# Kernel tuning notes

Measured on AMD Instinct MI355X. Metric: run time of the kernel, lower is better.

## Reference

```python
import jax, jax.numpy as jnp
import numpy as np

THRESHOLD = 0.2
NEG_POS_RATIO = 3
ALPHA = 1.0
B, M, P, C = 64, 50, 24564, 2


def cxcy_to_xy(c):
    return jnp.concatenate([c[..., :2] - c[..., 2:] / 2, c[..., :2] + c[..., 2:] / 2], axis=-1)


def xy_to_cxcy(x):
    return jnp.concatenate([(x[..., :2] + x[..., 2:]) / 2, x[..., 2:] - x[..., :2]], axis=-1)


def cxcy_to_gcxgcy(c, p):
    # SSD encoding: offsets scaled by 10, sizes (log) scaled by 5
    return jnp.concatenate([(c[..., :2] - p[..., :2]) / (p[..., 2:] / 10.0),
                            jnp.log(c[..., 2:] / p[..., 2:]) * 5.0], axis=-1)


def jaccard(a, b):
    # a: (M,4) xy boxes, b: (P,4) xy boxes -> (M,P) IoU
    lt = jnp.maximum(a[:, None, :2], b[None, :, :2])
    rb = jnp.minimum(a[:, None, 2:], b[None, :, 2:])
    inter = jnp.prod(jnp.clip(rb - lt, 0.0), axis=-1)
    area_a = jnp.prod(a[:, 2:] - a[:, :2], axis=-1)
    area_b = jnp.prod(b[:, 2:] - b[:, :2], axis=-1)
    return inter / (area_a[:, None] + area_b[None, :] - inter)


def setup_inputs() -> dict:
    key = jax.random.key(0)
    k1, k2, k3, k4, k5, k6 = jax.random.split(key, 6)
    predicted_locs = jax.random.normal(k1, (B, P, 4), dtype=jnp.float32)
    predicted_scores = jax.random.normal(k2, (B, P, C), dtype=jnp.float32)
    # valid GT corner boxes in [0,1]: x2>x1, y2>y1
    xy1 = jax.random.uniform(k3, (B, M, 2), minval=0.0, maxval=0.75)
    wh = jax.random.uniform(k4, (B, M, 2), minval=0.05, maxval=0.25)
    boxes = jnp.concatenate([xy1, xy1 + wh], axis=-1).astype(jnp.float32)
    # priors in cxcywh with positive sizes
    pc = jax.random.uniform(k5, (P, 2), minval=0.0, maxval=1.0)
    pwh = jax.random.uniform(k6, (P, 2), minval=0.02, maxval=0.3)
    priors_cxcy = jnp.concatenate([pc, pwh], axis=-1).astype(jnp.float32)
    return {"predicted_locs": predicted_locs, "predicted_scores": predicted_scores,
            "boxes": boxes, "priors_cxcy": priors_cxcy}


def reference(predicted_locs, predicted_scores, boxes, priors_cxcy):
    n_priors = priors_cxcy.shape[0]
    priors_xy = cxcy_to_xy(priors_cxcy)

    def assign(boxes_i):  # boxes_i: (M,4) xy
        overlap = jaccard(boxes_i, priors_xy)  # (M,P)
        overlap_for_each_prior = overlap.max(axis=0)        # (P,)
        object_for_each_prior = overlap.argmax(axis=0)      # (P,)
        prior_for_each_object = overlap.argmax(axis=1)      # (M,)
        # force each object's best prior to be assigned to that object
        object_for_each_prior = object_for_each_prior.at[prior_for_each_object].set(jnp.arange(boxes_i.shape[0]))
        overlap_for_each_prior = overlap_for_each_prior.at[prior_for_each_object].set(1.0)
        labels = jnp.where(overlap_for_each_prior < THRESHOLD, 0, 1).astype(jnp.int32)
        true_locs = cxcy_to_gcxgcy(xy_to_cxcy(boxes_i[object_for_each_prior]), priors_cxcy)
        return labels, true_locs

    true_classes, true_locs = jax.vmap(assign)(boxes)  # (B,P), (B,P,4)
    pos = true_classes != 0                            # (B,P)
    n_pos = pos.sum(axis=1)                            # (B,)
    total_pos = n_pos.sum().astype(jnp.float32)

    # L1Loss(mean) over the positive-prior coordinates
    loc_abs = jnp.abs(predicted_locs - true_locs)
    loc_loss = jnp.sum(loc_abs * pos[..., None]) / (total_pos * 4.0)

    # per-prior cross entropy
    logp = jax.nn.log_softmax(predicted_scores, axis=-1)
    conf_all = -jnp.take_along_axis(logp, true_classes[..., None].astype(jnp.int32), axis=-1)[..., 0]  # (B,P)
    conf_pos_sum = jnp.sum(conf_all * pos)

    # hard negative mining: zero positives, sort descending, take top 3*n_pos per image
    conf_neg = jnp.where(pos, 0.0, conf_all)
    conf_neg_sorted = -jnp.sort(-conf_neg, axis=1)
    ranks = jnp.arange(n_priors)[None, :]
    hard = ranks < (NEG_POS_RATIO * n_pos)[:, None]
    conf_hard_sum = jnp.sum(conf_neg_sorted * hard)

    conf_loss = (conf_hard_sum + conf_pos_sum) / total_pos
    return conf_loss + ALPHA * loc_loss
```

## Files before the change

kernel.cpp:

```cpp
#include <hip/hip_runtime.h>
#include <math.h>

#define BB 64
#define MM 50
#define PP 24564
#define NBLK 96
#define THRESH 0.2f
#define P4 (PP / 4)
#define SLACK 64u
#define NCH 24
#define WMARG 0.151f
#define RCPM 8u
#define SELCH 8
#define SCH4 ((P4 + SELCH - 1) / SELCH)
#define CAP PP

__device__ __forceinline__ float l1loc(float4 bxm, float4 pc, float4 pl) {
    float cx = (bxm.x + bxm.z) * 0.5f, cy = (bxm.y + bxm.w) * 0.5f;
    float w = bxm.z - bxm.x, h = bxm.w - bxm.y;
    float g0 = (cx - pc.x) / (pc.z * 0.1f);
    float g1 = (cy - pc.y) / (pc.w * 0.1f);
    float g2 = logf(w / pc.z) * 5.0f;
    float g3 = logf(h / pc.w) * 5.0f;
    return fabsf(pl.x - g0) + fabsf(pl.y - g1) + fabsf(pl.z - g2) + fabsf(pl.w - g3);
}

__global__ void k_init(int* __restrict__ ghist, int* __restrict__ ghist2,
                       int* __restrict__ gcur, unsigned long long* __restrict__ Lm) {
    int i = blockIdx.x * 256 + threadIdx.x;
    if (i < BB * 2048) ghist[i] = 0;
    if (i < BB * 1024) ghist2[i] = 0;
    if (i < BB) gcur[i] = 0;
    if (i < BB * MM) Lm[i] = 0x00000000FFFFFFFFull;
}

__global__ void k_main(const float4* __restrict__ boxes,
                       const float4* __restrict__ pr_cxcy,
                       const float4* __restrict__ plocs,
                       const float2* __restrict__ scores,
                       unsigned long long* __restrict__ Lm,
                       float* __restrict__ bestv,
                       int* __restrict__ bmv,
                       float* __restrict__ confneg,
                       int* __restrict__ ghist,
                       int* __restrict__ npos_part,
                       float* __restrict__ cpos_part,
                       float* __restrict__ loc_part) {
    int b = blockIdx.y;
    int p = blockIdx.x * 256 + threadIdx.x;
    int tid = threadIdx.x;
    __shared__ unsigned long long smax[MM];
    __shared__ int shist[2048];
    __shared__ int si[256];
    __shared__ float s1[256], s2[256];
    for (int i = tid; i < 2048; i += 256) shist[i] = 0;
    if (tid < MM) smax[tid] = 0ull;
    __syncthreads();

    const float4* boxb = boxes + b * MM;
    int np = 0;
    float cpos = 0.0f, lloc = 0.0f;
    if (p < PP) {
        float4 pc = pr_cxcy[p];
        float px1 = pc.x - pc.z * 0.5f, py1 = pc.y - pc.w * 0.5f;
        float px2 = pc.x + pc.z * 0.5f, py2 = pc.y + pc.w * 0.5f;
        float pa = (px2 - px1) * (py2 - py1);
        float binter = 0.0f, bdenom = 1.0f;
        int bm = 0;
        float4 bbm = boxb[0];
        #pragma unroll 5
        for (int m = 0; m < MM; ++m) {
            float4 bxm = boxb[m];
            float am = (bxm.z - bxm.x) * (bxm.w - bxm.y);
            float lx = fmaxf(bxm.x, px1), ly = fmaxf(bxm.y, py1);
            float rx = fminf(bxm.z, px2), ry = fminf(bxm.w, py2);
            float iw = fmaxf(rx - lx, 0.0f), ih = fmaxf(ry - ly, 0.0f);
            float inter = iw * ih;
            float den = am + pa - inter;
            float l = inter * bdenom, r = binter * den;
            if (l > r) { binter = inter; bdenom = den; bm = m; bbm = bxm; }
        }
        float q = binter / bdenom;
        size_t idx = (size_t)b * PP + p;
        bestv[idx] = q;
        bmv[idx] = bm;
        unsigned long long key =
            ((unsigned long long)__float_as_uint(q) << 32) | (unsigned int)(~p);
        atomicMax(&smax[bm], key);
        bool pos = (q >= THRESH);
        float2 sc = scores[idx];
        float mx = fmaxf(sc.x, sc.y);
        float lse = mx + logf(expf(sc.x - mx) + expf(sc.y - mx));
        float conf = pos ? (lse - sc.y) : (lse - sc.x);
        float ck = pos ? 0.0f : conf;
        confneg[idx] = ck;
        atomicAdd(&shist[__float_as_uint(ck) >> 20], 1);
        if (pos) {
            np = 1;
            cpos = conf;
            lloc = l1loc(bbm, pc, plocs[idx]);
        }
    }
    si[tid] = np; s1[tid] = cpos; s2[tid] = lloc;
    __syncthreads();
    for (int s = 128; s > 0; s >>= 1) {
        if (tid < s) {
            si[tid] += si[tid + s];
            s1[tid] += s1[tid + s];
            s2[tid] += s2[tid + s];
        }
        __syncthreads();
    }
    if (tid == 0) {
        int o = b * NBLK + blockIdx.x;
        npos_part[o] = si[0];
        cpos_part[o] = s1[0];
        loc_part[o] = s2[0];
    }
    if (tid < MM) {
        unsigned long long v = smax[tid];
        if (v) atomicMax(&Lm[b * MM + tid], v);
    }
    for (int i = tid; i < 2048; i += 256) {
        int c = shist[i];
        if (c) atomicAdd(&ghist[b * 2048 + i], c);
    }
}

__global__ void k_bpo3(const float4* __restrict__ boxes,
                       const float4* __restrict__ pr_cxcy,
                       const float* __restrict__ bestv,
                       unsigned long long* __restrict__ Lm) {
    int b = blockIdx.y, c = blockIdx.x, tid = threadIdx.x;
    __shared__ unsigned thr[MM];
    __shared__ unsigned long long smax[MM];
    __shared__ unsigned sminthr;
    if (tid < MM) {
        unsigned long long L = Lm[b * MM + tid];
        smax[tid] = L;
        unsigned hi = (unsigned)(L >> 32);
        thr[tid] = (hi > SLACK) ? hi - SLACK : 0u;
    }
    __syncthreads();
    if (tid == 0) {
        unsigned mt = 0xFFFFFFFFu;
        for (int j = 0; j < MM; ++j) mt = min(mt, thr[j]);
        sminthr = mt;
    }
    __syncthreads();
    unsigned minthr = sminthr;
    volatile unsigned long long* vsm = smax;
    const float4* boxb = boxes + b * MM;
    const float4* bv4 = (const float4*)(bestv + (size_t)b * PP);
    int i = c * 256 + tid;
    if (i < P4) {
        float4 qv = bv4[i];
        float vv[4] = {qv.x, qv.y, qv.z, qv.w};
        #pragma unroll
        for (int e = 0; e < 4; ++e) {
            unsigned qb = __float_as_uint(vv[e]);
            if (qb < minthr) continue;
            int p = 4 * i + e;
            float4 pc = pr_cxcy[p];
            float px1 = pc.x - pc.z * 0.5f, py1 = pc.y - pc.w * 0.5f;
            float px2 = pc.x + pc.z * 0.5f, py2 = pc.y + pc.w * 0.5f;
            float pa = (px2 - px1) * (py2 - py1);
            for (int j = 0; j < MM; ++j) {
                if (qb < thr[j]) continue;
                float4 bxm = boxb[j];
                if (pc.x < bxm.x - WMARG || pc.x > bxm.z + WMARG ||
                    pc.y < bxm.y - WMARG || pc.y > bxm.w + WMARG) continue;
                float am = (bxm.z - bxm.x) * (bxm.w - bxm.y);
                float lx = fmaxf(bxm.x, px1), ly = fmaxf(bxm.y, py1);
                float rx = fminf(bxm.z, px2), ry = fminf(bxm.w, py2);
                float iw = fmaxf(rx - lx, 0.0f), ih = fmaxf(ry - ly, 0.0f);
                float inter = iw * ih;
                float den = am + pa - inter;
                float qa = inter * __builtin_amdgcn_rcpf(den);
                unsigned hi = (unsigned)(vsm[j] >> 32);
                if (__float_as_uint(qa) + RCPM < hi) continue;
                float q = inter / den;
                unsigned long long key =
                    ((unsigned long long)__float_as_uint(q) << 32) | (unsigned int)(~p);
                if (key > vsm[j]) atomicMax(&smax[j], key);
            }
        }
    }
    __syncthreads();
    if (tid < MM) atomicMax(&Lm[b * MM + tid], smax[tid]);
}

__device__ __forceinline__ float block_sum(float v, float* fred, int tid) {
    fred[tid] = v;
    __syncthreads();
    for (int s = 128; s > 0; s >>= 1) {
        if (tid < s) fred[tid] += fred[tid + s];
        __syncthreads();
    }
    float r = fred[0];
    __syncthreads();
    return r;
}

template <int NB>
__device__ __forceinline__ void suffix_find(const int* __restrict__ h, int K, int tid,
                                            int* iscr, int* bcast, int slot) {
    const int c = NB / 256;
    const int base = tid * c;
    int tsum = 0;
    #pragma unroll
    for (int i = 0; i < c; ++i) tsum += h[base + i];
    iscr[tid] = tsum;
    __syncthreads();
    int val = tsum;
    for (int off = 1; off < 256; off <<= 1) {
        int other = (tid + off < 256) ? iscr[tid + off] : 0;
        __syncthreads();
        val += other;
        iscr[tid] = val;
        __syncthreads();
    }
    int acc = val - tsum;
    int best = -1, cg = 0;
    for (int i = base + c - 1; i >= base; --i) {
        int s = acc + h[i];
        if (s >= K) { best = i; cg = acc; break; }
        acc = s;
    }
    iscr[tid] = best;
    __syncthreads();
    for (int s2 = 128; s2 > 0; s2 >>= 1) {
        if (tid < s2) iscr[tid] = max(iscr[tid], iscr[tid + s2]);
        __syncthreads();
    }
    int gbest = iscr[0];
    __syncthreads();
    if (best == gbest && best >= 0) { bcast[slot] = gbest; bcast[slot + 1] = cg; }
    __syncthreads();
}

__global__ void k_selKF(const float4* __restrict__ boxes,
                        const float4* __restrict__ pr_cxcy,
                        const float4* __restrict__ plocs,
                        const float2* __restrict__ scores,
                        const unsigned long long* __restrict__ Lm,
                        const float* __restrict__ bestv,
                        const int* __restrict__ bmv,
                        float* __restrict__ confneg,
                        const int* __restrict__ ghist,
                        const int* __restrict__ npos_part,
                        int4* __restrict__ selp,
                        int* __restrict__ npfix,
                        float* __restrict__ cposfix,
                        float* __restrict__ llocfix) {
    int b = blockIdx.x, tid = threadIdx.x;
    __shared__ int h[2048];
    __shared__ int iscr[256];
    __shared__ int bcast[8];
    __shared__ int s_dnp;
    for (int i = tid; i < 2048; i += 256) h[i] = ghist[b * 2048 + i];
    __syncthreads();
    if (tid < 64) {
        int fp = -1;
        if (tid < MM) fp = (int)(~(unsigned)(Lm[b * MM + tid] & 0xFFFFFFFFull));
        bool active = (tid < MM);
        for (int m2 = 0; m2 < MM; ++m2) {
            int v = __shfl(fp, m2);
            if (m2 > tid && v == fp) active = false;
        }
        int dnp = 0;
        float dcp = 0.0f, dll = 0.0f;
        if (active) {
            size_t idx = (size_t)b * PP + fp;
            float bo = bestv[idx];
            bool npold = (bo >= THRESH);
            float4 pc = pr_cxcy[fp];
            float4 pl = plocs[idx];
            float llnew = l1loc(boxes[b * MM + tid], pc, pl);
            if (npold) {
                dll = llnew - l1loc(boxes[b * MM + bmv[idx]], pc, pl);
            } else {
                float2 sc = scores[idx];
                float mx = fmaxf(sc.x, sc.y);
                float lse = mx + logf(expf(sc.x - mx) + expf(sc.y - mx));
                dnp = 1;
                dcp = lse - sc.y;
                dll = llnew;
                float cold = confneg[idx];
                atomicAdd(&h[(int)(__float_as_uint(cold) >> 20)], -1);
                atomicAdd(&h[0], 1);
                confneg[idx] = 0.0f;
            }
        }
        #pragma unroll
        for (int off = 32; off > 0; off >>= 1) {
            dnp += __shfl_xor(dnp, off);
            dcp += __shfl_xor(dcp, off);
            dll += __shfl_xor(dll, off);
        }
        if (tid == 0) {
            s_dnp = dnp;
            npfix[b] = dnp; cposfix[b] = dcp; llocfix[b] = dll;
        }
    }
    __syncthreads();
    iscr[tid] = (tid < NBLK) ? npos_part[b * NBLK + tid] : 0;
    __syncthreads();
    for (int s = 128; s > 0; s >>= 1) {
        if (tid < s) iscr[tid] += iscr[tid + s];
        __syncthreads();
    }
    int npos = iscr[0] + s_dnp;
    __syncthreads();
    long long Kl = 3LL * npos;
    int K = (Kl > PP) ? PP : (int)Kl;
    if (K == 0) {
        if (tid == 0) selp[b] = make_int4(0, -1, 0, 0);
        return;
    }
    suffix_find<2048>(h, K, tid, iscr, bcast, 0);
    if (tid == 0) {
        int b1 = bcast[0];
        selp[b] = make_int4(K, b1, K - bcast[1], h[b1]);
    }
}

__global__ void k_selA(const float* __restrict__ confneg,
                       const int4* __restrict__ selp,
                       float* __restrict__ saP,
                       int* __restrict__ ghist2,
                       int* __restrict__ gcur,
                       float* __restrict__ gstore) {
    int b = blockIdx.y, c = blockIdx.x, tid = threadIdx.x;
    __shared__ float fred[256];
    __shared__ int h2[1024];
    __shared__ float sstore[SCH4 * 4];
    __shared__ int scnt, sbase;
    for (int i = tid; i < 1024; i += 256) h2[i] = 0;
    if (tid == 0) scnt = 0;
    __syncthreads();
    int4 sp = selp[b];
    int b1 = sp.y;
    float sa = 0.0f;
    if (b1 >= 0) {
        const float4* cn4 = (const float4*)(confneg + (size_t)b * PP);
        int i1 = min((c + 1) * SCH4, P4);
        for (int i = c * SCH4 + tid; i < i1; i += 256) {
            float4 q = cn4[i];
            float vv[4] = {q.x, q.y, q.z, q.w};
            #pragma unroll
            for (int j = 0; j < 4; ++j) {
                unsigned k = __float_as_uint(vv[j]);
                int t11 = (int)(k >> 20);
                if (t11 > b1) sa += vv[j];
                else if (t11 == b1) {
                    atomicAdd(&h2[(k >> 10) & 1023], 1);
                    int ix = atomicAdd(&scnt, 1);
                    sstore[ix] = vv[j];
                }
            }
        }
    }
    __syncthreads();
    if (tid == 0 && scnt > 0) sbase = atomicAdd(&gcur[b], scnt);
    __syncthreads();
    int n = scnt;
    for (int i = tid; i < n; i += 256)
        gstore[(size_t)b * CAP + sbase + i] = sstore[i];
    for (int i = tid; i < 1024; i += 256) {
        int v = h2[i];
        if (v) atomicAdd(&ghist2[b * 1024 + i], v);
    }
    float Sa = block_sum(sa, fred, tid);
    if (tid == 0) saP[b * SELCH + c] = Sa;
}

__global__ void k_selB(const int4* __restrict__ selp,
                       const float* __restrict__ saP,
                       const int* __restrict__ ghist2,
                       const float* __restrict__ gstore,
                       float* __restrict__ chard) {
    int b = blockIdx.x, tid = threadIdx.x;
    __shared__ int h[1024];
    __shared__ float fred[256];
    __shared__ int iscr[256];
    __shared__ int bcast[8];
    __shared__ float sSa;
    int4 sp = selp[b];
    if (sp.x == 0) {
        if (tid == 0) chard[b] = 0.0f;
        return;
    }
    int b1 = sp.y, K1 = sp.z, h1cnt = sp.w;
    if (tid == 0) {
        float s = 0.0f;
        for (int j = 0; j < SELCH; ++j) s += saP[b * SELCH + j];
        sSa = s;
    }
    for (int i = tid; i < 1024; i += 256) h[i] = ghist2[b * 1024 + i];
    __syncthreads();
    float Sa = sSa;
    suffix_find<1024>(h, K1, tid, iscr, bcast, 0);
    int b2 = bcast[0];
    int K2 = K1 - bcast[1];
    unsigned top21 = ((unsigned)b1 << 10) | (unsigned)b2;
    __syncthreads();

    const float* gs = gstore + (size_t)b * CAP;
    for (int i = tid; i < 1024; i += 256) h[i] = 0;
    __syncthreads();
    float sb = 0.0f;
    for (int i = tid; i < h1cnt; i += 256) {
        float v = gs[i];
        unsigned k = __float_as_uint(v);
        int n10 = (int)((k >> 10) & 1023);
        if (n10 > b2) sb += v;
        else if (n10 == b2) atomicAdd(&h[k & 1023], 1);
    }
    float Sb = block_sum(sb, fred, tid);
    suffix_find<1024>(h, K2, tid, iscr, bcast, 2);
    int b3 = bcast[2];
    int K3 = K2 - bcast[3];
    float sc = 0.0f;
    for (int i = tid; i < h1cnt; i += 256) {
        float v = gs[i];
        unsigned k = __float_as_uint(v);
        if ((k >> 10) == top21 && (k & 1023) > (unsigned)b3) sc += v;
    }
    float Sc = block_sum(sc, fred, tid);
    if (tid == 0) {
        unsigned kstar = (top21 << 10) | (unsigned)b3;
        chard[b] = Sa + Sb + Sc + (float)K3 * __uint_as_float(kstar);
    }
}

__global__ void k_final(const int* __restrict__ npos_part,
                        const float* __restrict__ cpos_part,
                        const float* __restrict__ loc_part,
                        const float* __restrict__ chard,
                        const int* __restrict__ npfix,
                        const float* __restrict__ cposfix,
                        const float* __restrict__ llocfix,
                        float* __restrict__ out) {
    __shared__ int si[256];
    __shared__ float s1[256], s2[256], s3[256];
    int tn = 0; float tc = 0.0f, tl = 0.0f, th = 0.0f;
    for (int i = threadIdx.x; i < BB * NBLK; i += 256) {
        tn += npos_part[i];
        tc += cpos_part[i];
        tl += loc_part[i];
    }
    if (threadIdx.x < BB) {
        th = chard[threadIdx.x];
        tn += npfix[threadIdx.x];
        tc += cposfix[threadIdx.x];
        tl += llocfix[threadIdx.x];
    }
    si[threadIdx.x] = tn; s1[threadIdx.x] = tc; s2[threadIdx.x] = tl; s3[threadIdx.x] = th;
    __syncthreads();
    for (int s = 128; s > 0; s >>= 1) {
        if (threadIdx.x < s) {
            si[threadIdx.x] += si[threadIdx.x + s];
            s1[threadIdx.x] += s1[threadIdx.x + s];
            s2[threadIdx.x] += s2[threadIdx.x + s];
            s3[threadIdx.x] += s3[threadIdx.x + s];
        }
        __syncthreads();
    }
    if (threadIdx.x == 0) {
        float tp = (float)si[0];
        out[0] = (s3[0] + s1[0]) / tp + s2[0] / (tp * 4.0f);
    }
}

extern "C" void kernel_launch(void* const* d_in, const int* in_sizes, int n_in,
                              void* d_out, int out_size, void* d_ws, size_t ws_size,
                              hipStream_t stream) {
    const float4* plocs   = (const float4*)d_in[0];
    const float2* scores  = (const float2*)d_in[1];
    const float4* boxes   = (const float4*)d_in[2];
    const float4* priors  = (const float4*)d_in[3];
    float* out = (float*)d_out;

    char* ws = (char*)d_ws;
    size_t off = 0;
    auto alloc = [&](size_t bytes) -> void* {
        void* p = ws + off;
        off += (bytes + 255) & ~(size_t)255;
        return p;
    };
    float*              confneg = (float*) alloc((size_t)BB * PP * 4);
    float*              bestv   = (float*) alloc((size_t)BB * PP * 4);
    int*                bmv     = (int*)   alloc((size_t)BB * PP * 4);
    int*                ghist   = (int*)   alloc((size_t)BB * 2048 * 4);
    int*                ghist2  = (int*)   alloc((size_t)BB * 1024 * 4);
    unsigned long long* Lm      = (unsigned long long*)alloc((size_t)BB * MM * 8);
    int*                npos_p  = (int*)   alloc((size_t)BB * NBLK * 4);
    float*              cpos_p  = (float*) alloc((size_t)BB * NBLK * 4);
    float*              loc_p   = (float*) alloc((size_t)BB * NBLK * 4);
    float*              chard   = (float*) alloc((size_t)BB * 4);
    int*                npfix   = (int*)   alloc((size_t)BB * 4);
    float*              cposfix = (float*) alloc((size_t)BB * 4);
    float*              llocfix = (float*) alloc((size_t)BB * 4);
    int4*               selp    = (int4*)  alloc((size_t)BB * 16);
    float*              saP     = (float*) alloc((size_t)BB * SELCH * 4);
    int*                gcur    = (int*)   alloc((size_t)BB * 4);
    float*              gstore  = (float*) alloc((size_t)BB * CAP * 4);
    (void)ws_size; (void)in_sizes; (void)n_in; (void)out_size;

    k_init<<<512, 256, 0, stream>>>(ghist, ghist2, gcur, Lm);
    k_main<<<dim3(NBLK, BB), 256, 0, stream>>>(boxes, priors, plocs, scores,
                                               Lm, bestv, bmv, confneg, ghist,
                                               npos_p, cpos_p, loc_p);
    k_bpo3<<<dim3(NCH, BB), 256, 0, stream>>>(boxes, priors, bestv, Lm);
    k_selKF<<<BB, 256, 0, stream>>>(boxes, priors, plocs, scores, Lm, bestv, bmv,
                                    confneg, ghist, npos_p, selp,
                                    npfix, cposfix, llocfix);
    k_selA<<<dim3(SELCH, BB), 256, 0, stream>>>(confneg, selp, saP, ghist2, gcur, gstore);
    k_selB<<<BB, 256, 0, stream>>>(selp, saP, ghist2, gstore, chard);
    k_final<<<1, 256, 0, stream>>>(npos_p, cpos_p, loc_p, chard,
                                   npfix, cposfix, llocfix, out);
}
```

Before: 156.2 us.

## Cache GT boxes in LDS and sort thresholds for early-exit prior-object search

Both the IoU-assignment kernel and the per-object best-prior kernel now stage the image's GT boxes and their areas in shared memory instead of re-reading global memory each iteration. The second kernel sorts per-object thresholds by rank and computes a wavefront-wide max of the best-overlap values. A wave can then skip entirely, and each prior's object loop can break early once thresholds exceed that max. This trades some setup work (an O(M^2) rank sort and a shuffle reduction) for less divergent looping and fewer global box loads.

```diff
diff --git a/kernel.cpp b/kernel.cpp
--- a/kernel.cpp
+++ b/kernel.cpp
@@ -49,15 +49,21 @@
     int b = blockIdx.y;
     int p = blockIdx.x * 256 + threadIdx.x;
     int tid = threadIdx.x;
+    __shared__ float4 sbox[MM];
+    __shared__ float sarea[MM];
     __shared__ unsigned long long smax[MM];
     __shared__ int shist[2048];
     __shared__ int si[256];
     __shared__ float s1[256], s2[256];
     for (int i = tid; i < 2048; i += 256) shist[i] = 0;
-    if (tid < MM) smax[tid] = 0ull;
-    __syncthreads();
-
-    const float4* boxb = boxes + b * MM;
+    if (tid < MM) {
+        float4 bxt = boxes[b * MM + tid];
+        sbox[tid] = bxt;
+        sarea[tid] = (bxt.z - bxt.x) * (bxt.w - bxt.y);
+        smax[tid] = 0ull;
+    }
+    __syncthreads();
+
     int np = 0;
     float cpos = 0.0f, lloc = 0.0f;
     if (p < PP) {
@@ -67,18 +73,15 @@
         float pa = (px2 - px1) * (py2 - py1);
         float binter = 0.0f, bdenom = 1.0f;
         int bm = 0;
-        float4 bbm = boxb[0];
-        #pragma unroll 5
         for (int m = 0; m < MM; ++m) {
-            float4 bxm = boxb[m];
-            float am = (bxm.z - bxm.x) * (bxm.w - bxm.y);
+            float4 bxm = sbox[m];
             float lx = fmaxf(bxm.x, px1), ly = fmaxf(bxm.y, py1);
             float rx = fminf(bxm.z, px2), ry = fminf(bxm.w, py2);
             float iw = fmaxf(rx - lx, 0.0f), ih = fmaxf(ry - ly, 0.0f);
             float inter = iw * ih;
-            float den = am + pa - inter;
+            float den = sarea[m] + pa - inter;
             float l = inter * bdenom, r = binter * den;
-            if (l > r) { binter = inter; bdenom = den; bm = m; bbm = bxm; }
+            if (l > r) { binter = inter; bdenom = den; bm = m; }
         }
         float q = binter / bdenom;
         size_t idx = (size_t)b * PP + p;
@@ -98,7 +101,7 @@
         if (pos) {
             np = 1;
             cpos = conf;
-            lloc = l1loc(bbm, pc, plocs[idx]);
+            lloc = l1loc(sbox[bm], pc, plocs[idx]);
         }
     }
     si[tid] = np; s1[tid] = cpos; s2[tid] = lloc;
@@ -132,50 +135,69 @@
                        const float* __restrict__ bestv,
                        unsigned long long* __restrict__ Lm) {
     int b = blockIdx.y, c = blockIdx.x, tid = threadIdx.x;
+    __shared__ float4 sbox[MM];
+    __shared__ float sarea[MM];
     __shared__ unsigned thr[MM];
+    __shared__ unsigned thrs[MM];
+    __shared__ unsigned char order[MM];
     __shared__ unsigned long long smax[MM];
-    __shared__ unsigned sminthr;
     if (tid < MM) {
+        float4 bxt = boxes[b * MM + tid];
+        sbox[tid] = bxt;
+        sarea[tid] = (bxt.z - bxt.x) * (bxt.w - bxt.y);
         unsigned long long L = Lm[b * MM + tid];
         smax[tid] = L;
         unsigned hi = (unsigned)(L >> 32);
         thr[tid] = (hi > SLACK) ? hi - SLACK : 0u;
     }
     __syncthreads();
-    if (tid == 0) {
-        unsigned mt = 0xFFFFFFFFu;
-        for (int j = 0; j < MM; ++j) mt = min(mt, thr[j]);
-        sminthr = mt;
-    }
-    __syncthreads();
-    unsigned minthr = sminthr;
+    if (tid < MM) {
+        unsigned tj = thr[tid];
+        int rank = 0;
+        for (int k = 0; k < MM; ++k) {
+            unsigned tk = thr[k];
+            if (tk < tj || (tk == tj && k < tid)) rank++;
+        }
+        order[rank] = (unsigned char)tid;
+        thrs[rank] = tj;
+    }
+    __syncthreads();
+    unsigned minthr = thrs[0];
     volatile unsigned long long* vsm = smax;
-    const float4* boxb = boxes + b * MM;
     const float4* bv4 = (const float4*)(bestv + (size_t)b * PP);
     int i = c * 256 + tid;
+    unsigned qb4[4] = {0u, 0u, 0u, 0u};
     if (i < P4) {
         float4 qv = bv4[i];
-        float vv[4] = {qv.x, qv.y, qv.z, qv.w};
+        qb4[0] = __float_as_uint(qv.x); qb4[1] = __float_as_uint(qv.y);
+        qb4[2] = __float_as_uint(qv.z); qb4[3] = __float_as_uint(qv.w);
+    }
+    unsigned wqb = max(max(qb4[0], qb4[1]), max(qb4[2], qb4[3]));
+    #pragma unroll
+    for (int off = 32; off > 0; off >>= 1)
+        wqb = max(wqb, (unsigned)__shfl_xor((int)wqb, off));
+    if (i < P4 && wqb >= minthr) {
         #pragma unroll
         for (int e = 0; e < 4; ++e) {
-            unsigned qb = __float_as_uint(vv[e]);
+            unsigned qb = qb4[e];
             if (qb < minthr) continue;
             int p = 4 * i + e;
             float4 pc = pr_cxcy[p];
             float px1 = pc.x - pc.z * 0.5f, py1 = pc.y - pc.w * 0.5f;
             float px2 = pc.x + pc.z * 0.5f, py2 = pc.y + pc.w * 0.5f;
             float pa = (px2 - px1) * (py2 - py1);
-            for (int j = 0; j < MM; ++j) {
-                if (qb < thr[j]) continue;
-                float4 bxm = boxb[j];
+            for (int jj = 0; jj < MM; ++jj) {
+                if (thrs[jj] > wqb) break;
+                if (qb < thrs[jj]) continue;
+                int j = (int)order[jj];
+                float4 bxm = sbox[j];
                 if (pc.x < bxm.x - WMARG || pc.x > bxm.z + WMARG ||
                     pc.y < bxm.y - WMARG || pc.y > bxm.w + WMARG) continue;
-                float am = (bxm.z - bxm.x) * (bxm.w - bxm.y);
                 float lx = fmaxf(bxm.x, px1), ly = fmaxf(bxm.y, py1);
                 float rx = fminf(bxm.z, px2), ry = fminf(bxm.w, py2);
                 float iw = fmaxf(rx - lx, 0.0f), ih = fmaxf(ry - ly, 0.0f);
                 float inter = iw * ih;
-                float den = am + pa - inter;
+                float den = sarea[j] + pa - inter;
                 float qa = inter * __builtin_amdgcn_rcpf(den);
                 unsigned hi = (unsigned)(vsm[j] >> 32);
                 if (__float_as_uint(qa) + RCPM < hi) continue;
```

Measured after the change: 161.6 us. 3.4% more time.
